# Kernel tuning notes

Measured on AMD Instinct MI355X. Metric: run time of the kernel, lower is better.

The kernel has to match this reference:

```python
import jax, jax.numpy as jnp
import numpy as np

N, E, G = 50000, 1600000, 64
D_IN, D_EDGE, D_H, D_U, D_OUT = 32, 32, 64, 16, 32


def _linear_params(key, d_in, d_out):
    kw, kb = jax.random.split(key)
    lim = 1.0 / np.sqrt(d_in)
    W = jax.random.uniform(kw, (d_in, d_out), minval=-lim, maxval=lim, dtype=jnp.float32)
    b = jax.random.uniform(kb, (d_out,), minval=-lim, maxval=lim, dtype=jnp.float32)
    return W, b


def setup_inputs() -> dict:
    key = jax.random.key(0)
    ks = jax.random.split(key, 10)
    x = jax.random.normal(ks[0], (N, D_IN), dtype=jnp.float32)
    edge_index = jax.random.randint(ks[1], (2, E), 0, N, dtype=jnp.int64)
    edge_attr = jax.random.normal(ks[2], (E, D_EDGE), dtype=jnp.float32)
    u = jax.random.normal(ks[3], (G, D_U), dtype=jnp.float32)
    batch = jnp.sort(jax.random.randint(ks[4], (N,), 0, G, dtype=jnp.int64))
    W1a, b1a = _linear_params(ks[5], D_IN + D_EDGE, D_H)   # node linear 0
    W1b, b1b = _linear_params(ks[6], D_H, D_H)             # node linear 1 (hidden)
    W2a, b2a = _linear_params(ks[7], D_IN + D_H + D_U, D_H)
    W2b, b2b = _linear_params(ks[8], D_H, D_OUT)
    return dict(x=x, edge_index=edge_index, edge_attr=edge_attr, u=u, batch=batch,
                W1a=W1a, b1a=b1a, W1b=W1b, b1b=b1b,
                W2a=W2a, b2a=b2a, W2b=W2b, b2b=b2b)


def reference(x, edge_index, edge_attr, u, batch,
              W1a, b1a, W1b, b1b, W2a, b2a, W2b, b2b):
    row, col = edge_index[0], edge_index[1]
    # edge-level MLP on [x[col] || edge_attr]
    h = jnp.concatenate([x[col], edge_attr], axis=1)          # [E, D_IN+D_EDGE]
    h = jax.nn.relu(h @ W1a + b1a)                            # [E, D_H]
    h = jax.nn.relu(h @ W1b + b1b)                            # [E, D_H]
    # scatter_mean over destination nodes (row), dim_size = N
    summed = jax.ops.segment_sum(h, row, num_segments=N)      # [N, D_H]
    counts = jax.ops.segment_sum(jnp.ones((h.shape[0],), h.dtype), row, num_segments=N)
    agg = summed / jnp.maximum(counts, 1.0)[:, None]
    # node-level MLP on [x || agg || u[batch]]
    z = jnp.concatenate([x, agg, u[batch]], axis=1)           # [N, D_IN+D_H+D_U]
    z = jax.nn.relu(z @ W2a + b2a)
    return z @ W2b + b2b                                      # [N, D_OUT]
```

## Files before the change

kernel.cpp:

```cpp
#include <hip/hip_runtime.h>
#include <hip/hip_bf16.h>


typedef __attribute__((ext_vector_type(8))) short bf16x8;
typedef __attribute__((ext_vector_type(4))) float f32x4;

__device__ __forceinline__ unsigned short f2bf(float f) {
    union { float f; unsigned u; } v; v.f = f;
    return (unsigned short)((v.u + 0x7FFFu + ((v.u >> 16) & 1u)) >> 16);
}


__global__ __launch_bounds__(256) void count_rows(
    const int* __restrict__ erow, int* __restrict__ counts, int E)
{
    const int gid = blockIdx.x * blockDim.x + threadIdx.x;
    const int stride = gridDim.x * blockDim.x;
    const int n4 = E >> 2;
    for (int i = gid; i < n4; i += stride) {
        const int4 r = ((const int4*)erow)[i];
        atomicAdd(&counts[r.x], 1);
        atomicAdd(&counts[r.y], 1);
        atomicAdd(&counts[r.z], 1);
        atomicAdd(&counts[r.w], 1);
    }
    for (int i = (n4 << 2) + gid; i < E; i += stride)
        atomicAdd(&counts[erow[i]], 1);
}

__global__ __launch_bounds__(256) void scan_blocks(
    const int* __restrict__ counts, int* __restrict__ excl,
    int* __restrict__ bsum, int N)
{
    __shared__ int tmp[256];
    const int t = threadIdx.x;
    const int i = blockIdx.x * 256 + t;
    const int v = (i < N) ? counts[i] : 0;
    tmp[t] = v; __syncthreads();
#pragma unroll
    for (int o = 1; o < 256; o <<= 1) {
        const int a = (t >= o) ? tmp[t - o] : 0;
        __syncthreads();
        tmp[t] += a;
        __syncthreads();
    }
    if (i < N) excl[i] = tmp[t] - v;
    if (t == 255) bsum[blockIdx.x] = tmp[t];
}

__global__ __launch_bounds__(256) void scan_bsum(int* __restrict__ bsum, int nb)
{
    __shared__ int tmp[256];
    const int t = threadIdx.x;
    const int v = (t < nb) ? bsum[t] : 0;
    tmp[t] = v; __syncthreads();
#pragma unroll
    for (int o = 1; o < 256; o <<= 1) {
        const int a = (t >= o) ? tmp[t - o] : 0;
        __syncthreads();
        tmp[t] += a;
        __syncthreads();
    }
    if (t < nb) bsum[t] = tmp[t] - v;
}

__global__ __launch_bounds__(256) void scan_add(
    int* __restrict__ rowstart, const int* __restrict__ bsum, int N, int E)
{
    const int i = blockIdx.x * 256 + threadIdx.x;
    if (i < N) rowstart[i] += bsum[blockIdx.x];
    if (i == 0) rowstart[N] = E;
}

__global__ __launch_bounds__(256) void permute_edges(
    const int* __restrict__ erow, const int* __restrict__ ecol,
    int* __restrict__ cursor, int4* __restrict__ sorted4, int E)
{
    const int gid = blockIdx.x * blockDim.x + threadIdx.x;
    const int stride = gridDim.x * blockDim.x;
    const int n4 = E >> 2;
    for (int i = gid; i < n4; i += stride) {
        const int4 r = ((const int4*)erow)[i];
        const int4 c = ((const int4*)ecol)[i];
        const int e0 = i << 2;
        int pos;
        pos = atomicAdd(&cursor[r.x], 1); sorted4[pos] = int4{e0,     c.x, r.x, 0};
        pos = atomicAdd(&cursor[r.y], 1); sorted4[pos] = int4{e0 + 1, c.y, r.y, 0};
        pos = atomicAdd(&cursor[r.z], 1); sorted4[pos] = int4{e0 + 2, c.z, r.z, 0};
        pos = atomicAdd(&cursor[r.w], 1); sorted4[pos] = int4{e0 + 3, c.w, r.w, 0};
    }
    for (int i = (n4 << 2) + gid; i < E; i += stride) {
        const int r = erow[i];
        const int pos = atomicAdd(&cursor[r], 1);
        sorted4[pos] = int4{i, ecol[i], r, 0};
    }
}


__global__ __launch_bounds__(256, 3) void edge_mlp_mfma(
    const float* __restrict__ x,
    const int4*  __restrict__ sorted4,
    const float* __restrict__ eattr,
    const float* __restrict__ W1a,
    const float* __restrict__ b1a,
    const float* __restrict__ W1b,
    const float* __restrict__ b1b,
    float* __restrict__ summed,
    int E)
{
    __shared__ __align__(16) unsigned short H2[4 * 16 * 64];

    const int tid  = threadIdx.x;
    const int lane = tid & 63;
    const int wv   = tid >> 6;
    const int g    = lane >> 4;
    const int el   = lane & 15;

    unsigned short* const h2w = H2 + wv * (16 * 64);

    bf16x8 wa[4][2], wb[4][2];
    f32x4  bias1[4];
    float  bias2s[4];
#pragma unroll
    for (int mt = 0; mt < 4; ++mt) {
        const int o = mt * 16 + el;
#pragma unroll
        for (int ks = 0; ks < 2; ++ks) {
            bf16x8 ta, tb;
#pragma unroll
            for (int j = 0; j < 8; ++j) {
                const int k = ks * 32 + 8 * g + j;
                ta[j] = (short)f2bf(W1a[k * 64 + o]);
                tb[j] = (short)f2bf(W1b[k * 64 + o]);
            }
            wa[mt][ks] = ta;
            wb[mt][ks] = tb;
        }
#pragma unroll
        for (int r = 0; r < 4; ++r) bias1[mt][r] = b1a[mt * 16 + 4 * g + r];
        bias2s[mt] = b1b[o];
    }

    const int ntile = (E + 15) >> 4;
    const int wid   = blockIdx.x * 4 + wv;
    const int nw    = gridDim.x * 4;

    const int sw = el & 7;

    for (int t = wid; t < ntile; t += nw) {
        const int ebase = t << 4;

        int4 s4;
        if (ebase + el < E) s4 = sorted4[ebase + el];
        else                s4 = int4{0, 0, -1, 0};
        const int row = s4.z;

        bf16x8 bf0, bf1;
        {
            const float4* xp = (const float4*)(x + (size_t)s4.y * 32 + 8 * g);
            const float4* ap = (const float4*)(eattr + (size_t)s4.x * 32 + 8 * g);
            const float4 x0 = xp[0], x1 = xp[1];
            const float4 a0v = ap[0], a1v = ap[1];
            bf0[0] = (short)f2bf(x0.x); bf0[1] = (short)f2bf(x0.y);
            bf0[2] = (short)f2bf(x0.z); bf0[3] = (short)f2bf(x0.w);
            bf0[4] = (short)f2bf(x1.x); bf0[5] = (short)f2bf(x1.y);
            bf0[6] = (short)f2bf(x1.z); bf0[7] = (short)f2bf(x1.w);
            bf1[0] = (short)f2bf(a0v.x); bf1[1] = (short)f2bf(a0v.y);
            bf1[2] = (short)f2bf(a0v.z); bf1[3] = (short)f2bf(a0v.w);
            bf1[4] = (short)f2bf(a1v.x); bf1[5] = (short)f2bf(a1v.y);
            bf1[6] = (short)f2bf(a1v.z); bf1[7] = (short)f2bf(a1v.w);
        }

        f32x4 a0 = bias1[0], a1 = bias1[1], a2 = bias1[2], a3 = bias1[3];
        a0 = __builtin_amdgcn_mfma_f32_16x16x32_bf16(wa[0][0], bf0, a0, 0, 0, 0);
        a1 = __builtin_amdgcn_mfma_f32_16x16x32_bf16(wa[1][0], bf0, a1, 0, 0, 0);
        a2 = __builtin_amdgcn_mfma_f32_16x16x32_bf16(wa[2][0], bf0, a2, 0, 0, 0);
        a3 = __builtin_amdgcn_mfma_f32_16x16x32_bf16(wa[3][0], bf0, a3, 0, 0, 0);
        a0 = __builtin_amdgcn_mfma_f32_16x16x32_bf16(wa[0][1], bf1, a0, 0, 0, 0);
        a1 = __builtin_amdgcn_mfma_f32_16x16x32_bf16(wa[1][1], bf1, a1, 0, 0, 0);
        a2 = __builtin_amdgcn_mfma_f32_16x16x32_bf16(wa[2][1], bf1, a2, 0, 0, 0);
        a3 = __builtin_amdgcn_mfma_f32_16x16x32_bf16(wa[3][1], bf1, a3, 0, 0, 0);

        unsigned short* hrow = h2w + el * 64;
        {
            f32x4 accs[4] = {a0, a1, a2, a3};
#pragma unroll
            for (int mt = 0; mt < 4; ++mt) {
                unsigned short pk[4];
#pragma unroll
                for (int r = 0; r < 4; ++r) pk[r] = f2bf(fmaxf(accs[mt][r], 0.f));
                const int hid   = mt * 16 + 4 * g;
                const int chunk = hid >> 3;
                const int off   = hid & 7;
                *(uint2*)(hrow + ((chunk ^ sw) * 8 + off)) = *(uint2*)pk;
            }
        }

        const bf16x8 hb0 = *(const bf16x8*)(hrow + (((0 + g) ^ sw) * 8));
        const bf16x8 hb1 = *(const bf16x8*)(hrow + (((4 + g) ^ sw) * 8));
        f32x4 d0 = {bias2s[0], bias2s[0], bias2s[0], bias2s[0]};
        f32x4 d1 = {bias2s[1], bias2s[1], bias2s[1], bias2s[1]};
        f32x4 d2 = {bias2s[2], bias2s[2], bias2s[2], bias2s[2]};
        f32x4 d3 = {bias2s[3], bias2s[3], bias2s[3], bias2s[3]};
        d0 = __builtin_amdgcn_mfma_f32_16x16x32_bf16(hb0, wb[0][0], d0, 0, 0, 0);
        d1 = __builtin_amdgcn_mfma_f32_16x16x32_bf16(hb0, wb[1][0], d1, 0, 0, 0);
        d2 = __builtin_amdgcn_mfma_f32_16x16x32_bf16(hb0, wb[2][0], d2, 0, 0, 0);
        d3 = __builtin_amdgcn_mfma_f32_16x16x32_bf16(hb0, wb[3][0], d3, 0, 0, 0);
        d0 = __builtin_amdgcn_mfma_f32_16x16x32_bf16(hb1, wb[0][1], d0, 0, 0, 0);
        d1 = __builtin_amdgcn_mfma_f32_16x16x32_bf16(hb1, wb[1][1], d1, 0, 0, 0);
        d2 = __builtin_amdgcn_mfma_f32_16x16x32_bf16(hb1, wb[2][1], d2, 0, 0, 0);
        d3 = __builtin_amdgcn_mfma_f32_16x16x32_bf16(hb1, wb[3][1], d3, 0, 0, 0);

#pragma unroll
        for (int r = 0; r < 4; ++r) {
            d0[r] = fmaxf(d0[r], 0.f);
            d1[r] = fmaxf(d1[r], 0.f);
            d2[r] = fmaxf(d2[r], 0.f);
            d3[r] = fmaxf(d3[r], 0.f);
        }

        const int prevrow = __shfl(row, lane - 1);
        unsigned long long bmask =
            __ballot((g == 0) && (el > 0) && (row != prevrow));
        bmask = (bmask & 0xFFFEull) | 0x10000ull;

        int s = 0;
        while (s < 16) {
            const int e = s + 1 + (__ffsll(bmask >> (s + 1)) - 1);
            const int rowid = __shfl(row, s);
            if (rowid >= 0) {
                float s0 = 0.f, s1 = 0.f, s2 = 0.f, s3 = 0.f;
#pragma unroll
                for (int r = 0; r < 4; ++r) {
                    const int ej = 4 * g + r;
                    const bool in = (ej >= s) && (ej < e);
                    s0 += in ? d0[r] : 0.f;
                    s1 += in ? d1[r] : 0.f;
                    s2 += in ? d2[r] : 0.f;
                    s3 += in ? d3[r] : 0.f;
                }
                s0 += __shfl_xor(s0, 16); s0 += __shfl_xor(s0, 32);
                s1 += __shfl_xor(s1, 16); s1 += __shfl_xor(s1, 32);
                s2 += __shfl_xor(s2, 16); s2 += __shfl_xor(s2, 32);
                s3 += __shfl_xor(s3, 16); s3 += __shfl_xor(s3, 32);
                const float val = (g == 0) ? s0 : (g == 1) ? s1
                                : (g == 2) ? s2 : s3;
                unsafeAtomicAdd(&summed[(size_t)rowid * 64 + lane], val);
            }
            s = e;
        }
    }
}


__global__ __launch_bounds__(256, 2) void node_mlp_mfma(
    const float* __restrict__ x,
    const float* __restrict__ summed,
    const int*   __restrict__ rowstart,
    const float* __restrict__ u,
    const int*   __restrict__ batch,
    const float* __restrict__ W2a,
    const float* __restrict__ b2a,
    const float* __restrict__ W2b,
    const float* __restrict__ b2b,
    float* __restrict__ out,
    int N)
{
    __shared__ __align__(16) unsigned short In[64 * 128];
    __shared__ __align__(16) unsigned short H[64 * 64];

    const int tid  = threadIdx.x;
    const int lane = tid & 63;
    const int wv   = tid >> 6;
    const int g    = lane >> 4;
    const int el   = lane & 15;

    bf16x8 wa[4][4];
    f32x4  bias1[4];
#pragma unroll
    for (int mt = 0; mt < 4; ++mt) {
        const int o = mt * 16 + el;
#pragma unroll
        for (int ks = 0; ks < 4; ++ks) {
            bf16x8 ta;
#pragma unroll
            for (int j = 0; j < 8; ++j) {
                const int k = ks * 32 + 8 * g + j;
                ta[j] = (k < 112) ? (short)f2bf(W2a[k * 64 + o]) : (short)0;
            }
            wa[mt][ks] = ta;
        }
#pragma unroll
        for (int r = 0; r < 4; ++r) bias1[mt][r] = b2a[mt * 16 + 4 * g + r];
    }
    bf16x8 wb[2][2];
    float  bias2s[2];
#pragma unroll
    for (int nt = 0; nt < 2; ++nt) {
        const int o = nt * 16 + el;
#pragma unroll
        for (int ks = 0; ks < 2; ++ks) {
            bf16x8 tb;
#pragma unroll
            for (int j = 0; j < 8; ++j) {
                const int k = ks * 32 + 8 * g + j;
                tb[j] = (short)f2bf(W2b[k * 32 + o]);
            }
            wb[nt][ks] = tb;
        }
        bias2s[nt] = b2b[o];
    }

    unsigned short* const inrow = In + (wv * 16) * 128;
    unsigned short* const hrow0 = H + (wv * 16) * 64;

    const int ntile = (N + 15) >> 4;
    const int wid   = blockIdx.x * 4 + wv;
    const int nw    = gridDim.x * 4;

    for (int t = wid; t < ntile; t += nw) {
        const int nbase = t << 4;

        {
            const int le = lane >> 2;
            const int p  = lane & 3;
            const int n  = nbase + le;
            float4 v[8];
            if (n < N) {
                if (p == 0) {
                    const float4* xp = (const float4*)(x + (size_t)n * 32);
#pragma unroll
                    for (int q = 0; q < 8; ++q) v[q] = xp[q];
                } else if (p < 3) {
                    const int cnt = rowstart[n + 1] - rowstart[n];
                    const float inv = 1.0f / fmaxf((float)cnt, 1.0f);
                    const float4* sp = (const float4*)(summed + (size_t)n * 64 + (p - 1) * 32);
#pragma unroll
                    for (int q = 0; q < 8; ++q) {
                        v[q] = sp[q];
                        v[q].x *= inv; v[q].y *= inv; v[q].z *= inv; v[q].w *= inv;
                    }
                } else {
                    const int gb = batch[n];
                    const float4* up = (const float4*)(u + (size_t)gb * 16);
#pragma unroll
                    for (int q = 0; q < 4; ++q) v[q] = up[q];
#pragma unroll
                    for (int q = 4; q < 8; ++q) v[q] = float4{0.f, 0.f, 0.f, 0.f};
                }
            } else {
#pragma unroll
                for (int q = 0; q < 8; ++q) v[q] = float4{0.f, 0.f, 0.f, 0.f};
            }
            const int sw = le & 7;
            unsigned short* row = inrow + le * 128;
#pragma unroll
            for (int q = 0; q < 4; ++q) {
                bf16x8 c;
                const float4 va = v[2 * q], vb = v[2 * q + 1];
                c[0] = (short)f2bf(va.x); c[1] = (short)f2bf(va.y);
                c[2] = (short)f2bf(va.z); c[3] = (short)f2bf(va.w);
                c[4] = (short)f2bf(vb.x); c[5] = (short)f2bf(vb.y);
                c[6] = (short)f2bf(vb.z); c[7] = (short)f2bf(vb.w);
                const int cc = 4 * p + q;
                const int ci = (cc & 8) | ((cc & 7) ^ sw);
                *(bf16x8*)(row + ci * 8) = c;
            }
        }

        const unsigned short* brow = inrow + el * 128;
        const int sw7 = el & 7;
        f32x4 a0 = bias1[0], a1 = bias1[1], a2 = bias1[2], a3 = bias1[3];
#pragma unroll
        for (int ks = 0; ks < 4; ++ks) {
            const int cc = ks * 4 + g;
            const int ci = (cc & 8) | ((cc & 7) ^ sw7);
            const bf16x8 bf = *(const bf16x8*)(brow + ci * 8);
            a0 = __builtin_amdgcn_mfma_f32_16x16x32_bf16(wa[0][ks], bf, a0, 0, 0, 0);
            a1 = __builtin_amdgcn_mfma_f32_16x16x32_bf16(wa[1][ks], bf, a1, 0, 0, 0);
            a2 = __builtin_amdgcn_mfma_f32_16x16x32_bf16(wa[2][ks], bf, a2, 0, 0, 0);
            a3 = __builtin_amdgcn_mfma_f32_16x16x32_bf16(wa[3][ks], bf, a3, 0, 0, 0);
        }

        unsigned short* hrow = hrow0 + el * 64;
        {
            f32x4 accs[4] = {a0, a1, a2, a3};
#pragma unroll
            for (int mt = 0; mt < 4; ++mt) {
                unsigned short pk[4];
#pragma unroll
                for (int r = 0; r < 4; ++r) pk[r] = f2bf(fmaxf(accs[mt][r], 0.f));
                const int hid   = mt * 16 + 4 * g;
                const int chunk = hid >> 3;
                const int off   = hid & 7;
                *(uint2*)(hrow + ((chunk ^ sw7) * 8 + off)) = *(uint2*)pk;
            }
        }

        const bf16x8 hb0 = *(const bf16x8*)(hrow + (((0 + g) ^ sw7) * 8));
        const bf16x8 hb1 = *(const bf16x8*)(hrow + (((4 + g) ^ sw7) * 8));
        f32x4 dn0 = {bias2s[0], bias2s[0], bias2s[0], bias2s[0]};
        f32x4 dn1 = {bias2s[1], bias2s[1], bias2s[1], bias2s[1]};
        dn0 = __builtin_amdgcn_mfma_f32_16x16x32_bf16(hb0, wb[0][0], dn0, 0, 0, 0);
        dn1 = __builtin_amdgcn_mfma_f32_16x16x32_bf16(hb0, wb[1][0], dn1, 0, 0, 0);
        dn0 = __builtin_amdgcn_mfma_f32_16x16x32_bf16(hb1, wb[0][1], dn0, 0, 0, 0);
        dn1 = __builtin_amdgcn_mfma_f32_16x16x32_bf16(hb1, wb[1][1], dn1, 0, 0, 0);

        if (nbase + 16 <= N) {
#pragma unroll
            for (int r = 0; r < 4; ++r) {
                float* dst = out + (size_t)(nbase + 4 * g + r) * 32 + el;
                dst[0]  = dn0[r];
                dst[16] = dn1[r];
            }
        } else {
#pragma unroll
            for (int r = 0; r < 4; ++r) {
                const int n = nbase + 4 * g + r;
                if (n < N) {
                    float* dst = out + (size_t)n * 32 + el;
                    dst[0]  = dn0[r];
                    dst[16] = dn1[r];
                }
            }
        }
    }
}

extern "C" void kernel_launch(void* const* d_in, const int* in_sizes, int n_in,
                              void* d_out, int out_size, void* d_ws, size_t ws_size,
                              hipStream_t stream) {
    const float* x     = (const float*)d_in[0];
    const int*   eidx  = (const int*)d_in[1];
    const float* eattr = (const float*)d_in[2];
    const float* u     = (const float*)d_in[3];
    const int*   batch = (const int*)d_in[4];
    const float* W1a   = (const float*)d_in[5];
    const float* b1a   = (const float*)d_in[6];
    const float* W1b   = (const float*)d_in[7];
    const float* b1b   = (const float*)d_in[8];
    const float* W2a   = (const float*)d_in[9];
    const float* b2a   = (const float*)d_in[10];
    const float* W2b   = (const float*)d_in[11];
    const float* b2b   = (const float*)d_in[12];
    float* out = (float*)d_out;

    const int N = in_sizes[0] / 32;
    const int E = in_sizes[1] / 2;
    const int* erow = eidx;
    const int* ecol = eidx + E;

    int4*  sorted4  = (int4*)d_ws;
    float* summed   = (float*)(sorted4 + E);
    int*   counts   = (int*)(summed + (size_t)N * 64);
    int*   rowstart = counts + N;
    int*   cursor   = rowstart + (N + 1);
    int*   bsum     = cursor + N;

    hipMemsetAsync(summed, 0, ((size_t)N * 64 + N) * sizeof(float), stream);

    count_rows<<<1024, 256, 0, stream>>>(erow, counts, E);
    const int nb = (N + 255) / 256;
    scan_blocks<<<nb, 256, 0, stream>>>(counts, rowstart, bsum, N);
    scan_bsum<<<1, 256, 0, stream>>>(bsum, nb);
    scan_add<<<nb, 256, 0, stream>>>(rowstart, bsum, N, E);
    hipMemcpyAsync(cursor, rowstart, (size_t)N * sizeof(int),
                   hipMemcpyDeviceToDevice, stream);
    permute_edges<<<1024, 256, 0, stream>>>(erow, ecol, cursor, sorted4, E);

    edge_mlp_mfma<<<4096, 256, 0, stream>>>(x, sorted4, eattr,
                                            W1a, b1a, W1b, b1b, summed, E);
    node_mlp_mfma<<<784, 256, 0, stream>>>(x, summed, rowstart, u, batch,
                                           W2a, b2a, W2b, b2b, out, N);
}
```

Measured before the change: 335.0 us.

## Stage second-layer weights in LDS, raise occupancy, fuse cursor copy into scan_add

The second-layer W1b bf16 fragments move from per-thread registers into a shared-memory table that each wave reads during the MFMA step. This frees VGPRs so launch bounds can rise from 3 to 4 waves-per-EU blocks. The trade is extra LDS reads per tile and 8 KB more shared memory per block. Separately, scan_add now writes the cursor array itself, which removes a device-to-device memcpy.

```diff
diff --git a/kernel.cpp b/kernel.cpp
--- a/kernel.cpp
+++ b/kernel.cpp
@@ -65,10 +65,15 @@
 }
 
 __global__ __launch_bounds__(256) void scan_add(
-    int* __restrict__ rowstart, const int* __restrict__ bsum, int N, int E)
+    int* __restrict__ rowstart, int* __restrict__ cursor,
+    const int* __restrict__ bsum, int N, int E)
 {
     const int i = blockIdx.x * 256 + threadIdx.x;
-    if (i < N) rowstart[i] += bsum[blockIdx.x];
+    if (i < N) {
+        const int v = rowstart[i] + bsum[blockIdx.x];
+        rowstart[i] = v;
+        cursor[i]   = v;
+    }
     if (i == 0) rowstart[N] = E;
 }
 
@@ -97,7 +102,7 @@
 }
 
 
-__global__ __launch_bounds__(256, 3) void edge_mlp_mfma(
+__global__ __launch_bounds__(256, 4) void edge_mlp_mfma(
     const float* __restrict__ x,
     const int4*  __restrict__ sorted4,
     const float* __restrict__ eattr,
@@ -109,6 +114,7 @@
     int E)
 {
     __shared__ __align__(16) unsigned short H2[4 * 16 * 64];
+    __shared__ __align__(16) unsigned short WBL[512 * 8];
 
     const int tid  = threadIdx.x;
     const int lane = tid & 63;
@@ -118,7 +124,23 @@
 
     unsigned short* const h2w = H2 + wv * (16 * 64);
 
-    bf16x8 wa[4][2], wb[4][2];
+    for (int idx = tid; idx < 512; idx += 256) {
+        const int f  = idx >> 6;
+        const int l  = idx & 63;
+        const int gg = l >> 4;
+        const int ee = l & 15;
+        const int nt = f >> 1;
+        const int ks = f & 1;
+        const int o  = nt * 16 + ee;
+        bf16x8 v;
+#pragma unroll
+        for (int j = 0; j < 8; ++j)
+            v[j] = (short)f2bf(W1b[(ks * 32 + 8 * gg + j) * 64 + o]);
+        *(bf16x8*)(WBL + idx * 8) = v;
+    }
+    __syncthreads();
+
+    bf16x8 wa[4][2];
     f32x4  bias1[4];
     float  bias2s[4];
 #pragma unroll
@@ -126,15 +148,11 @@
         const int o = mt * 16 + el;
 #pragma unroll
         for (int ks = 0; ks < 2; ++ks) {
-            bf16x8 ta, tb;
-#pragma unroll
-            for (int j = 0; j < 8; ++j) {
-                const int k = ks * 32 + 8 * g + j;
-                ta[j] = (short)f2bf(W1a[k * 64 + o]);
-                tb[j] = (short)f2bf(W1b[k * 64 + o]);
-            }
+            bf16x8 ta;
+#pragma unroll
+            for (int j = 0; j < 8; ++j)
+                ta[j] = (short)f2bf(W1a[(ks * 32 + 8 * g + j) * 64 + o]);
             wa[mt][ks] = ta;
-            wb[mt][ks] = tb;
         }
 #pragma unroll
         for (int r = 0; r < 4; ++r) bias1[mt][r] = b1a[mt * 16 + 4 * g + r];
@@ -202,14 +220,17 @@
         f32x4 d1 = {bias2s[1], bias2s[1], bias2s[1], bias2s[1]};
         f32x4 d2 = {bias2s[2], bias2s[2], bias2s[2], bias2s[2]};
         f32x4 d3 = {bias2s[3], bias2s[3], bias2s[3], bias2s[3]};
-        d0 = __builtin_amdgcn_mfma_f32_16x16x32_bf16(hb0, wb[0][0], d0, 0, 0, 0);
-        d1 = __builtin_amdgcn_mfma_f32_16x16x32_bf16(hb0, wb[1][0], d1, 0, 0, 0);
-        d2 = __builtin_amdgcn_mfma_f32_16x16x32_bf16(hb0, wb[2][0], d2, 0, 0, 0);
-        d3 = __builtin_amdgcn_mfma_f32_16x16x32_bf16(hb0, wb[3][0], d3, 0, 0, 0);
-        d0 = __builtin_amdgcn_mfma_f32_16x16x32_bf16(hb1, wb[0][1], d0, 0, 0, 0);
-        d1 = __builtin_amdgcn_mfma_f32_16x16x32_bf16(hb1, wb[1][1], d1, 0, 0, 0);
-        d2 = __builtin_amdgcn_mfma_f32_16x16x32_bf16(hb1, wb[2][1], d2, 0, 0, 0);
-        d3 = __builtin_amdgcn_mfma_f32_16x16x32_bf16(hb1, wb[3][1], d3, 0, 0, 0);
+        {
+            const bf16x8* wbl = (const bf16x8*)WBL;
+            d0 = __builtin_amdgcn_mfma_f32_16x16x32_bf16(hb0, wbl[0 * 64 + lane], d0, 0, 0, 0);
+            d1 = __builtin_amdgcn_mfma_f32_16x16x32_bf16(hb0, wbl[2 * 64 + lane], d1, 0, 0, 0);
+            d2 = __builtin_amdgcn_mfma_f32_16x16x32_bf16(hb0, wbl[4 * 64 + lane], d2, 0, 0, 0);
+            d3 = __builtin_amdgcn_mfma_f32_16x16x32_bf16(hb0, wbl[6 * 64 + lane], d3, 0, 0, 0);
+            d0 = __builtin_amdgcn_mfma_f32_16x16x32_bf16(hb1, wbl[1 * 64 + lane], d0, 0, 0, 0);
+            d1 = __builtin_amdgcn_mfma_f32_16x16x32_bf16(hb1, wbl[3 * 64 + lane], d1, 0, 0, 0);
+            d2 = __builtin_amdgcn_mfma_f32_16x16x32_bf16(hb1, wbl[5 * 64 + lane], d2, 0, 0, 0);
+            d3 = __builtin_amdgcn_mfma_f32_16x16x32_bf16(hb1, wbl[7 * 64 + lane], d3, 0, 0, 0);
+        }
 
 #pragma unroll
         for (int r = 0; r < 4; ++r) {
@@ -463,9 +484,7 @@
     const int nb = (N + 255) / 256;
     scan_blocks<<<nb, 256, 0, stream>>>(counts, rowstart, bsum, N);
     scan_bsum<<<1, 256, 0, stream>>>(bsum, nb);
-    scan_add<<<nb, 256, 0, stream>>>(rowstart, bsum, N, E);
-    hipMemcpyAsync(cursor, rowstart, (size_t)N * sizeof(int),
-                   hipMemcpyDeviceToDevice, stream);
+    scan_add<<<nb, 256, 0, stream>>>(rowstart, cursor, bsum, N, E);
     permute_edges<<<1024, 256, 0, stream>>>(erow, ecol, cursor, sorted4, E);
 
     edge_mlp_mfma<<<4096, 256, 0, stream>>>(x, sorted4, eattr,
```

Result: slower. 410.9 us (+22.6%).

## Pack sorted edge records to int2 and process two edge tiles per wave

Applied to the files above, without the earlier changes.

Edge records written by the permute step shrink from int4 to int2 by packing column and row indices into 16 bits each, which halves the scatter-write and reload traffic. The separate device-to-device cursor copy is folded into scan_add. The edge MLP kernel now handles 32 edges per wave iteration, issuing all gathers for both 16-edge halves before computing, so more memory loads are in flight. Segment reduction spans both halves to merge runs of the same row and reduce atomics. The packing assumes node counts below 65536, and the extra live registers may lower occupancy.

```diff
diff --git a/kernel.cpp b/kernel.cpp
--- a/kernel.cpp
+++ b/kernel.cpp
@@ -65,16 +65,21 @@
 }
 
 __global__ __launch_bounds__(256) void scan_add(
-    int* __restrict__ rowstart, const int* __restrict__ bsum, int N, int E)
+    int* __restrict__ rowstart, int* __restrict__ cursor,
+    const int* __restrict__ bsum, int N, int E)
 {
     const int i = blockIdx.x * 256 + threadIdx.x;
-    if (i < N) rowstart[i] += bsum[blockIdx.x];
+    if (i < N) {
+        const int v = rowstart[i] + bsum[blockIdx.x];
+        rowstart[i] = v;
+        cursor[i]   = v;
+    }
     if (i == 0) rowstart[N] = E;
 }
 
 __global__ __launch_bounds__(256) void permute_edges(
     const int* __restrict__ erow, const int* __restrict__ ecol,
-    int* __restrict__ cursor, int4* __restrict__ sorted4, int E)
+    int* __restrict__ cursor, int2* __restrict__ sorted2, int E)
 {
     const int gid = blockIdx.x * blockDim.x + threadIdx.x;
     const int stride = gridDim.x * blockDim.x;
@@ -84,22 +89,26 @@
         const int4 c = ((const int4*)ecol)[i];
         const int e0 = i << 2;
         int pos;
-        pos = atomicAdd(&cursor[r.x], 1); sorted4[pos] = int4{e0,     c.x, r.x, 0};
-        pos = atomicAdd(&cursor[r.y], 1); sorted4[pos] = int4{e0 + 1, c.y, r.y, 0};
-        pos = atomicAdd(&cursor[r.z], 1); sorted4[pos] = int4{e0 + 2, c.z, r.z, 0};
-        pos = atomicAdd(&cursor[r.w], 1); sorted4[pos] = int4{e0 + 3, c.w, r.w, 0};
+        pos = atomicAdd(&cursor[r.x], 1);
+        sorted2[pos] = int2{e0,     (int)((unsigned)c.x | ((unsigned)r.x << 16))};
+        pos = atomicAdd(&cursor[r.y], 1);
+        sorted2[pos] = int2{e0 + 1, (int)((unsigned)c.y | ((unsigned)r.y << 16))};
+        pos = atomicAdd(&cursor[r.z], 1);
+        sorted2[pos] = int2{e0 + 2, (int)((unsigned)c.z | ((unsigned)r.z << 16))};
+        pos = atomicAdd(&cursor[r.w], 1);
+        sorted2[pos] = int2{e0 + 3, (int)((unsigned)c.w | ((unsigned)r.w << 16))};
     }
     for (int i = (n4 << 2) + gid; i < E; i += stride) {
         const int r = erow[i];
         const int pos = atomicAdd(&cursor[r], 1);
-        sorted4[pos] = int4{i, ecol[i], r, 0};
+        sorted2[pos] = int2{i, (int)((unsigned)ecol[i] | ((unsigned)r << 16))};
     }
 }
 
 
 __global__ __launch_bounds__(256, 3) void edge_mlp_mfma(
     const float* __restrict__ x,
-    const int4*  __restrict__ sorted4,
+    const int2*  __restrict__ sorted2,
     const float* __restrict__ eattr,
     const float* __restrict__ W1a,
     const float* __restrict__ b1a,
@@ -108,7 +117,7 @@
     float* __restrict__ summed,
     int E)
 {
-    __shared__ __align__(16) unsigned short H2[4 * 16 * 64];
+    __shared__ __align__(16) unsigned short H2[4 * 2 * 16 * 64];
 
     const int tid  = threadIdx.x;
     const int lane = tid & 63;
@@ -116,7 +125,8 @@
     const int g    = lane >> 4;
     const int el   = lane & 15;
 
-    unsigned short* const h2w = H2 + wv * (16 * 64);
+    unsigned short* const h2A = H2 + wv * (2 * 16 * 64);
+    unsigned short* const h2B = h2A + 16 * 64;
 
     bf16x8 wa[4][2], wb[4][2];
     f32x4  bias1[4];
@@ -141,35 +151,46 @@
         bias2s[mt] = b1b[o];
     }
 
-    const int ntile = (E + 15) >> 4;
+    const int ntile = (E + 31) >> 5;
     const int wid   = blockIdx.x * 4 + wv;
     const int nw    = gridDim.x * 4;
 
     const int sw = el & 7;
 
     for (int t = wid; t < ntile; t += nw) {
-        const int ebase = t << 4;
-
-        int4 s4;
-        if (ebase + el < E) s4 = sorted4[ebase + el];
-        else                s4 = int4{0, 0, -1, 0};
-        const int row = s4.z;
+        const int ebase = t << 5;
+
+        int2 sA, sB; int rowA, rowB;
+        if (ebase + el < E) {
+            sA = sorted2[ebase + el];
+            rowA = (int)((unsigned)sA.y >> 16);
+        } else { sA = int2{0, 0}; rowA = -1; }
+        if (ebase + 16 + el < E) {
+            sB = sorted2[ebase + 16 + el];
+            rowB = (int)((unsigned)sB.y >> 16);
+        } else { sB = int2{0, 0}; rowB = -1; }
+
+        float4 ax0, ax1, aa0, aa1, bx0, bx1, ba0, ba1;
+        {
+            const float4* xpA = (const float4*)(x + (size_t)(sA.y & 0xFFFF) * 32 + 8 * g);
+            const float4* apA = (const float4*)(eattr + (size_t)sA.x * 32 + 8 * g);
+            const float4* xpB = (const float4*)(x + (size_t)(sB.y & 0xFFFF) * 32 + 8 * g);
+            const float4* apB = (const float4*)(eattr + (size_t)sB.x * 32 + 8 * g);
+            ax0 = xpA[0]; ax1 = xpA[1];
+            aa0 = apA[0]; aa1 = apA[1];
+            bx0 = xpB[0]; bx1 = xpB[1];
+            ba0 = apB[0]; ba1 = apB[1];
+        }
 
         bf16x8 bf0, bf1;
-        {
-            const float4* xp = (const float4*)(x + (size_t)s4.y * 32 + 8 * g);
-            const float4* ap = (const float4*)(eattr + (size_t)s4.x * 32 + 8 * g);
-            const float4 x0 = xp[0], x1 = xp[1];
-            const float4 a0v = ap[0], a1v = ap[1];
-            bf0[0] = (short)f2bf(x0.x); bf0[1] = (short)f2bf(x0.y);
-            bf0[2] = (short)f2bf(x0.z); bf0[3] = (short)f2bf(x0.w);
-            bf0[4] = (short)f2bf(x1.x); bf0[5] = (short)f2bf(x1.y);
-            bf0[6] = (short)f2bf(x1.z); bf0[7] = (short)f2bf(x1.w);
-            bf1[0] = (short)f2bf(a0v.x); bf1[1] = (short)f2bf(a0v.y);
-            bf1[2] = (short)f2bf(a0v.z); bf1[3] = (short)f2bf(a0v.w);
-            bf1[4] = (short)f2bf(a1v.x); bf1[5] = (short)f2bf(a1v.y);
-            bf1[6] = (short)f2bf(a1v.z); bf1[7] = (short)f2bf(a1v.w);
-        }
+        bf0[0] = (short)f2bf(ax0.x); bf0[1] = (short)f2bf(ax0.y);
+        bf0[2] = (short)f2bf(ax0.z); bf0[3] = (short)f2bf(ax0.w);
+        bf0[4] = (short)f2bf(ax1.x); bf0[5] = (short)f2bf(ax1.y);
+        bf0[6] = (short)f2bf(ax1.z); bf0[7] = (short)f2bf(ax1.w);
+        bf1[0] = (short)f2bf(aa0.x); bf1[1] = (short)f2bf(aa0.y);
+        bf1[2] = (short)f2bf(aa0.z); bf1[3] = (short)f2bf(aa0.w);
+        bf1[4] = (short)f2bf(aa1.x); bf1[5] = (short)f2bf(aa1.y);
+        bf1[6] = (short)f2bf(aa1.z); bf1[7] = (short)f2bf(aa1.w);
 
         f32x4 a0 = bias1[0], a1 = bias1[1], a2 = bias1[2], a3 = bias1[3];
         a0 = __builtin_amdgcn_mfma_f32_16x16x32_bf16(wa[0][0], bf0, a0, 0, 0, 0);
@@ -181,7 +202,7 @@
         a2 = __builtin_amdgcn_mfma_f32_16x16x32_bf16(wa[2][1], bf1, a2, 0, 0, 0);
         a3 = __builtin_amdgcn_mfma_f32_16x16x32_bf16(wa[3][1], bf1, a3, 0, 0, 0);
 
-        unsigned short* hrow = h2w + el * 64;
+        unsigned short* hrowA = h2A + el * 64;
         {
             f32x4 accs[4] = {a0, a1, a2, a3};
 #pragma unroll
@@ -192,52 +213,108 @@
                 const int hid   = mt * 16 + 4 * g;
                 const int chunk = hid >> 3;
                 const int off   = hid & 7;
-                *(uint2*)(hrow + ((chunk ^ sw) * 8 + off)) = *(uint2*)pk;
-            }
-        }
-
-        const bf16x8 hb0 = *(const bf16x8*)(hrow + (((0 + g) ^ sw) * 8));
-        const bf16x8 hb1 = *(const bf16x8*)(hrow + (((4 + g) ^ sw) * 8));
-        f32x4 d0 = {bias2s[0], bias2s[0], bias2s[0], bias2s[0]};
-        f32x4 d1 = {bias2s[1], bias2s[1], bias2s[1], bias2s[1]};
-        f32x4 d2 = {bias2s[2], bias2s[2], bias2s[2], bias2s[2]};
-        f32x4 d3 = {bias2s[3], bias2s[3], bias2s[3], bias2s[3]};
-        d0 = __builtin_amdgcn_mfma_f32_16x16x32_bf16(hb0, wb[0][0], d0, 0, 0, 0);
-        d1 = __builtin_amdgcn_mfma_f32_16x16x32_bf16(hb0, wb[1][0], d1, 0, 0, 0);
-        d2 = __builtin_amdgcn_mfma_f32_16x16x32_bf16(hb0, wb[2][0], d2, 0, 0, 0);
-        d3 = __builtin_amdgcn_mfma_f32_16x16x32_bf16(hb0, wb[3][0], d3, 0, 0, 0);
-        d0 = __builtin_amdgcn_mfma_f32_16x16x32_bf16(hb1, wb[0][1], d0, 0, 0, 0);
-        d1 = __builtin_amdgcn_mfma_f32_16x16x32_bf16(hb1, wb[1][1], d1, 0, 0, 0);
-        d2 = __builtin_amdgcn_mfma_f32_16x16x32_bf16(hb1, wb[2][1], d2, 0, 0, 0);
-        d3 = __builtin_amdgcn_mfma_f32_16x16x32_bf16(hb1, wb[3][1], d3, 0, 0, 0);
+                *(uint2*)(hrowA + ((chunk ^ sw) * 8 + off)) = *(uint2*)pk;
+            }
+        }
+        const bf16x8 ha0 = *(const bf16x8*)(hrowA + (((0 + g) ^ sw) * 8));
+        const bf16x8 ha1 = *(const bf16x8*)(hrowA + (((4 + g) ^ sw) * 8));
+        f32x4 dA0 = {bias2s[0], bias2s[0], bias2s[0], bias2s[0]};
+        f32x4 dA1 = {bias2s[1], bias2s[1], bias2s[1], bias2s[1]};
+        f32x4 dA2 = {bias2s[2], bias2s[2], bias2s[2], bias2s[2]};
+        f32x4 dA3 = {bias2s[3], bias2s[3], bias2s[3], bias2s[3]};
+        dA0 = __builtin_amdgcn_mfma_f32_16x16x32_bf16(ha0, wb[0][0], dA0, 0, 0, 0);
+        dA1 = __builtin_amdgcn_mfma_f32_16x16x32_bf16(ha0, wb[1][0], dA1, 0, 0, 0);
+        dA2 = __builtin_amdgcn_mfma_f32_16x16x32_bf16(ha0, wb[2][0], dA2, 0, 0, 0);
+        dA3 = __builtin_amdgcn_mfma_f32_16x16x32_bf16(ha0, wb[3][0], dA3, 0, 0, 0);
+        dA0 = __builtin_amdgcn_mfma_f32_16x16x32_bf16(ha1, wb[0][1], dA0, 0, 0, 0);
+        dA1 = __builtin_amdgcn_mfma_f32_16x16x32_bf16(ha1, wb[1][1], dA1, 0, 0, 0);
+        dA2 = __builtin_amdgcn_mfma_f32_16x16x32_bf16(ha1, wb[2][1], dA2, 0, 0, 0);
+        dA3 = __builtin_amdgcn_mfma_f32_16x16x32_bf16(ha1, wb[3][1], dA3, 0, 0, 0);
+
+        bf16x8 cf0, cf1;
+        cf0[0] = (short)f2bf(bx0.x); cf0[1] = (short)f2bf(bx0.y);
+        cf0[2] = (short)f2bf(bx0.z); cf0[3] = (short)f2bf(bx0.w);
+        cf0[4] = (short)f2bf(bx1.x); cf0[5] = (short)f2bf(bx1.y);
+        cf0[6] = (short)f2bf(bx1.z); cf0[7] = (short)f2bf(bx1.w);
+        cf1[0] = (short)f2bf(ba0.x); cf1[1] = (short)f2bf(ba0.y);
+        cf1[2] = (short)f2bf(ba0.z); cf1[3] = (short)f2bf(ba0.w);
+        cf1[4] = (short)f2bf(ba1.x); cf1[5] = (short)f2bf(ba1.y);
+        cf1[6] = (short)f2bf(ba1.z); cf1[7] = (short)f2bf(ba1.w);
+
+        f32x4 b0 = bias1[0], b1 = bias1[1], b2 = bias1[2], b3 = bias1[3];
+        b0 = __builtin_amdgcn_mfma_f32_16x16x32_bf16(wa[0][0], cf0, b0, 0, 0, 0);
+        b1 = __builtin_amdgcn_mfma_f32_16x16x32_bf16(wa[1][0], cf0, b1, 0, 0, 0);
+        b2 = __builtin_amdgcn_mfma_f32_16x16x32_bf16(wa[2][0], cf0, b2, 0, 0, 0);
+        b3 = __builtin_amdgcn_mfma_f32_16x16x32_bf16(wa[3][0], cf0, b3, 0, 0, 0);
+        b0 = __builtin_amdgcn_mfma_f32_16x16x32_bf16(wa[0][1], cf1, b0, 0, 0, 0);
+        b1 = __builtin_amdgcn_mfma_f32_16x16x32_bf16(wa[1][1], cf1, b1, 0, 0, 0);
+        b2 = __builtin_amdgcn_mfma_f32_16x16x32_bf16(wa[2][1], cf1, b2, 0, 0, 0);
+        b3 = __builtin_amdgcn_mfma_f32_16x16x32_bf16(wa[3][1], cf1, b3, 0, 0, 0);
+
+        unsigned short* hrowB = h2B + el * 64;
+        {
+            f32x4 accs[4] = {b0, b1, b2, b3};
+#pragma unroll
+            for (int mt = 0; mt < 4; ++mt) {
+                unsigned short pk[4];
+#pragma unroll
+                for (int r = 0; r < 4; ++r) pk[r] = f2bf(fmaxf(accs[mt][r], 0.f));
+                const int hid   = mt * 16 + 4 * g;
+                const int chunk = hid >> 3;
+                const int off   = hid & 7;
+                *(uint2*)(hrowB + ((chunk ^ sw) * 8 + off)) = *(uint2*)pk;
+            }
+        }
+        const bf16x8 hb0 = *(const bf16x8*)(hrowB + (((0 + g) ^ sw) * 8));
+        const bf16x8 hb1 = *(const bf16x8*)(hrowB + (((4 + g) ^ sw) * 8));
+        f32x4 dB0 = {bias2s[0], bias2s[0], bias2s[0], bias2s[0]};
+        f32x4 dB1 = {bias2s[1], bias2s[1], bias2s[1], bias2s[1]};
+        f32x4 dB2 = {bias2s[2], bias2s[2], bias2s[2], bias2s[2]};
+        f32x4 dB3 = {bias2s[3], bias2s[3], bias2s[3], bias2s[3]};
+        dB0 = __builtin_amdgcn_mfma_f32_16x16x32_bf16(hb0, wb[0][0], dB0, 0, 0, 0);
+        dB1 = __builtin_amdgcn_mfma_f32_16x16x32_bf16(hb0, wb[1][0], dB1, 0, 0, 0);
+        dB2 = __builtin_amdgcn_mfma_f32_16x16x32_bf16(hb0, wb[2][0], dB2, 0, 0, 0);
+        dB3 = __builtin_amdgcn_mfma_f32_16x16x32_bf16(hb0, wb[3][0], dB3, 0, 0, 0);
+        dB0 = __builtin_amdgcn_mfma_f32_16x16x32_bf16(hb1, wb[0][1], dB0, 0, 0, 0);
+        dB1 = __builtin_amdgcn_mfma_f32_16x16x32_bf16(hb1, wb[1][1], dB1, 0, 0, 0);
+        dB2 = __builtin_amdgcn_mfma_f32_16x16x32_bf16(hb1, wb[2][1], dB2, 0, 0, 0);
+        dB3 = __builtin_amdgcn_mfma_f32_16x16x32_bf16(hb1, wb[3][1], dB3, 0, 0, 0);
 
 #pragma unroll
         for (int r = 0; r < 4; ++r) {
-            d0[r] = fmaxf(d0[r], 0.f);
-            d1[r] = fmaxf(d1[r], 0.f);
-            d2[r] = fmaxf(d2[r], 0.f);
-            d3[r] = fmaxf(d3[r], 0.f);
-        }
-
-        const int prevrow = __shfl(row, lane - 1);
-        unsigned long long bmask =
-            __ballot((g == 0) && (el > 0) && (row != prevrow));
-        bmask = (bmask & 0xFFFEull) | 0x10000ull;
+            dA0[r] = fmaxf(dA0[r], 0.f); dA1[r] = fmaxf(dA1[r], 0.f);
+            dA2[r] = fmaxf(dA2[r], 0.f); dA3[r] = fmaxf(dA3[r], 0.f);
+            dB0[r] = fmaxf(dB0[r], 0.f); dB1[r] = fmaxf(dB1[r], 0.f);
+            dB2[r] = fmaxf(dB2[r], 0.f); dB3[r] = fmaxf(dB3[r], 0.f);
+        }
+
+        const int prevA = __shfl(rowA, lane - 1);
+        unsigned long long mA = __ballot((g == 0) && (el > 0) && (rowA != prevA));
+        const int prevB = __shfl(rowB, lane - 1);
+        unsigned long long mB = __ballot((g == 0) && (el > 0) && (rowB != prevB));
+        const int lastA  = __shfl(rowA, 15);
+        const int firstB = __shfl(rowB, 0);
+        unsigned long long bmask = (mA & 0xFFFEull)
+                                 | ((mB & 0xFFFEull) << 16)
+                                 | ((unsigned long long)(firstB != lastA) << 16)
+                                 | (1ull << 32);
 
         int s = 0;
-        while (s < 16) {
+        while (s < 32) {
             const int e = s + 1 + (__ffsll(bmask >> (s + 1)) - 1);
-            const int rowid = __shfl(row, s);
+            const int rowid = (s < 16) ? __shfl(rowA, s) : __shfl(rowB, s - 16);
             if (rowid >= 0) {
                 float s0 = 0.f, s1 = 0.f, s2 = 0.f, s3 = 0.f;
 #pragma unroll
                 for (int r = 0; r < 4; ++r) {
-                    const int ej = 4 * g + r;
-                    const bool in = (ej >= s) && (ej < e);
-                    s0 += in ? d0[r] : 0.f;
-                    s1 += in ? d1[r] : 0.f;
-                    s2 += in ? d2[r] : 0.f;
-                    s3 += in ? d3[r] : 0.f;
+                    const int ejA = 4 * g + r;
+                    const int ejB = 16 + ejA;
+                    const bool inA = (ejA >= s) && (ejA < e);
+                    const bool inB = (ejB >= s) && (ejB < e);
+                    s0 += (inA ? dA0[r] : 0.f) + (inB ? dB0[r] : 0.f);
+                    s1 += (inA ? dA1[r] : 0.f) + (inB ? dB1[r] : 0.f);
+                    s2 += (inA ? dA2[r] : 0.f) + (inB ? dB2[r] : 0.f);
+                    s3 += (inA ? dA3[r] : 0.f) + (inB ? dB3[r] : 0.f);
                 }
                 s0 += __shfl_xor(s0, 16); s0 += __shfl_xor(s0, 32);
                 s1 += __shfl_xor(s1, 16); s1 += __shfl_xor(s1, 32);
@@ -450,8 +527,8 @@
     const int* erow = eidx;
     const int* ecol = eidx + E;
 
-    int4*  sorted4  = (int4*)d_ws;
-    float* summed   = (float*)(sorted4 + E);
+    int2*  sorted2  = (int2*)d_ws;
+    float* summed   = (float*)(sorted2 + E);
     int*   counts   = (int*)(summed + (size_t)N * 64);
     int*   rowstart = counts + N;
     int*   cursor   = rowstart + (N + 1);
@@ -463,12 +540,10 @@
     const int nb = (N + 255) / 256;
     scan_blocks<<<nb, 256, 0, stream>>>(counts, rowstart, bsum, N);
     scan_bsum<<<1, 256, 0, stream>>>(bsum, nb);
-    scan_add<<<nb, 256, 0, stream>>>(rowstart, bsum, N, E);
-    hipMemcpyAsync(cursor, rowstart, (size_t)N * sizeof(int),
-                   hipMemcpyDeviceToDevice, stream);
-    permute_edges<<<1024, 256, 0, stream>>>(erow, ecol, cursor, sorted4, E);
-
-    edge_mlp_mfma<<<4096, 256, 0, stream>>>(x, sorted4, eattr,
+    scan_add<<<nb, 256, 0, stream>>>(rowstart, cursor, bsum, N, E);
+    permute_edges<<<1024, 256, 0, stream>>>(erow, ecol, cursor, sorted2, E);
+
+    edge_mlp_mfma<<<4096, 256, 0, stream>>>(x, sorted2, eattr,
                                             W1a, b1a, W1b, b1b, summed, E);
     node_mlp_mfma<<<784, 256, 0, stream>>>(x, summed, rowstart, u, batch,
                                            W2a, b2a, W2b, b2b, out, N);
```

Measured after the change: 429.8 us. 1.28x slower.
